# Optimization experiments

Hardware: AMD Instinct MI355X
Metric: run time of the kernel (lower is better)

Reference implementation:

```python
import jax, jax.numpy as jnp
import numpy as np

KSIZE = 3
BJORCK_ITERS = 20
POWER_ITERS = 10


def _power_iteration_sigma(A, u):
    # A: [K, n, n], u: [K, n, 1] -> leading singular value per matrix, [K]
    for _ in range(POWER_ITERS):
        v = jnp.swapaxes(A, -1, -2) @ u
        v = v / jnp.linalg.norm(v, axis=-2, keepdims=True)
        u = A @ v
        u = u / jnp.linalg.norm(u, axis=-2, keepdims=True)
    s = (jnp.swapaxes(u, -1, -2) @ A @ v)[..., 0, 0]
    return s


def _bjorck(w, u):
    # power-iteration scaling is done under no_grad in torch -> stop_gradient
    s = jax.lax.stop_gradient(_power_iteration_sigma(jax.lax.stop_gradient(w), u))
    w = w / s[:, None, None]
    for _ in range(BJORCK_ITERS):
        wtw = jnp.swapaxes(w, -1, -2) @ w
        w = 1.5 * w - 0.5 * (w @ wtw)  # beta = 0.5, first order
    return w


def _block_orth(p1, p2):
    # -> [2, 2, n, n]
    n = p1.shape[0]
    I = jnp.eye(n, dtype=p1.dtype)
    return jnp.stack([
        jnp.stack([p1 @ p2, p1 @ (I - p2)]),
        jnp.stack([(I - p1) @ p2, (I - p1) @ (I - p2)]),
    ])


def _matrix_conv(m1, m2):
    # m1: [k,k,n,n], m2: [l,l,n,n] -> [k+l-1, k+l-1, n, n]
    k, l = m1.shape[0], m2.shape[0]
    size = k + l - 1
    rows = []
    for i in range(size):
        row = []
        for j in range(size):
            acc = 0.0
            for i1 in range(min(k, i + 1)):
                for j1 in range(min(k, j + 1)):
                    if i - i1 < l and j - j1 < l:
                        acc = acc + m1[i1, j1] @ m2[i - i1, j - j1]
            row.append(acc)
        rows.append(jnp.stack(row))
    return jnp.stack(rows)


def _bcop_weight(param_matrices, init_u):
    K, C, _ = param_matrices.shape  # K = 2*(KSIZE-1)+1, C = max_channels
    ortho = _bjorck(param_matrices, init_u)
    H = ortho[0]  # cin == cout == C, full slice
    half = C // 2
    mask = jnp.concatenate(
        [jnp.ones((K - 1, 1, half), ortho.dtype), jnp.zeros((K - 1, 1, C - half), ortho.dtype)],
        axis=-1)
    PQ = ortho[1:] * mask
    PQ = PQ @ jnp.swapaxes(PQ, -1, -2)  # symmetric projections [K-1, C, C]
    p = _block_orth(PQ[0], PQ[1])
    for t in range(1, KSIZE - 1):
        p = _matrix_conv(p, _block_orth(PQ[2 * t], PQ[2 * t + 1]))
    p = jnp.einsum('ab,ijbc->ijac', H, p)  # H @ p[i,j]
    # dict_to_tensor(...).permute(3, 2, 1, 0): [k, k, r, c] -> [c, r, j, i]
    return jnp.transpose(p, (3, 2, 1, 0))  # [C_out, C_in, KSIZE, KSIZE]


def setup_inputs() -> dict:
    key = jax.random.key(0)
    k1, k2, k3, k4 = jax.random.split(key, 4)
    C = 256
    num_kernels = 2 * (KSIZE - 1) + 1
    x = jax.random.normal(k1, (32, C, 64, 64), dtype=jnp.float32)
    param_matrices = jax.random.normal(k2, (num_kernels, C, C), dtype=jnp.float32) / np.sqrt(C)
    init_u = jax.random.normal(k3, (num_kernels, C, 1), dtype=jnp.float32)
    bias = jax.random.uniform(k4, (C,), dtype=jnp.float32, minval=-1.0 / np.sqrt(C), maxval=1.0 / np.sqrt(C))
    return {"x": x, "param_matrices": param_matrices, "init_u": init_u, "bias": bias}


def reference(x, param_matrices, init_u, bias):
    weight = _bcop_weight(param_matrices, init_u)
    # cyclic (circular) padding by k//2 on each side, odd kernel
    pad = KSIZE // 2
    xp = jnp.pad(x, ((0, 0), (0, 0), (pad, pad), (pad, pad)), mode='wrap')
    out = jax.lax.conv_general_dilated(
        xp, weight, window_strides=(1, 1), padding='VALID',
        dimension_numbers=('NCHW', 'OIHW', 'NCHW'))
    return out + bias[None, :, None, None]
```

## Files before the change

kernel.cpp:

```cpp
#include <hip/hip_runtime.h>
#include <stdint.h>

typedef unsigned short u16;
typedef unsigned short u16x4 __attribute__((ext_vector_type(4)));
typedef short bf16x8 __attribute__((ext_vector_type(8)));
typedef float f32x4 __attribute__((ext_vector_type(4)));

#define CDIM 256
#define MSZ 65536

constexpr size_t O_XB   = 0;
constexpr size_t O_AT   = 67108864;
constexpr size_t O_PQH  = 67108864;
constexpr size_t O_PQL  = O_PQH + 524288;
constexpr size_t O_SVAL = 68419584;
constexpr size_t O_W0   = 68419840;
constexpr size_t O_W1   = 71041280;
constexpr size_t O_PH   = 71041280;
constexpr size_t O_PL   = O_PH + 524288;
constexpr size_t O_QTH  = O_PL + 524288;
constexpr size_t O_QTL  = O_QTH + 524288;
constexpr size_t O_TH   = 73662720;
constexpr size_t O_TL   = O_TH + 655360;
constexpr size_t O_RTH  = 74973440;
constexpr size_t O_RTL  = O_RTH + 1179648;
constexpr size_t O_WBQ  = O_RTL + 1179648;

__device__ __forceinline__ u16 f2bf(float f) {
  union { float f; uint32_t u; } a; a.f = f;
  uint32_t u = a.u;
  uint32_t r = u + 0x7FFFu + ((u >> 16) & 1u);
  return (u16)(r >> 16);
}
__device__ __forceinline__ float bf2f(u16 u) {
  union { uint32_t u; float f; } a; a.u = ((uint32_t)u) << 16; return a.f;
}
__device__ __forceinline__ void split_st(u16* hi, u16* lo, float v) {
  u16 h = f2bf(v);
  *hi = h;
  *lo = f2bf(v - bf2f(h));
}
__device__ __forceinline__ void gl16(const void* g, void* l) {
  __builtin_amdgcn_global_load_lds(
      (const __attribute__((address_space(1))) void*)g,
      (__attribute__((address_space(3))) void*)l, 16, 0, 0);
}

__global__ void convert_k(const float* __restrict__ x, u16* __restrict__ xb) {
  __shared__ float t[32][33];
  int b = blockIdx.x;
  int ctile = b & 7, wtile = (b >> 3) & 1, h = (b >> 4) & 63, n = b >> 10;
  int c0 = ctile * 32, w0 = wtile * 32;
  int tid = threadIdx.x;
  for (int p = 0; p < 4; p++) {
    int e = tid + p * 256; int cc = e >> 5, ww = e & 31;
    t[cc][ww] = x[(((size_t)n * 256 + c0 + cc) * 64 + h) * 64 + w0 + ww];
  }
  __syncthreads();
  {
    int ww = tid >> 3, c4 = (tid & 7) * 4;
    u16x4 v;
    #pragma unroll
    for (int j = 0; j < 4; ++j) v[j] = f2bf(t[c4 + j][ww]);
    *(u16x4*)&xb[(((size_t)n * 64 + h) * 64 + w0 + ww) * 256 + c0 + c4] = v;
  }
}

__global__ void wtwA_k(const float* __restrict__ W, float* __restrict__ T) {
  int m = blockIdx.y;
  int i0 = (blockIdx.x >> 3) * 32, j0 = (blockIdx.x & 7) * 32;
  const float* A = W + (size_t)m * MSZ;
  __shared__ float As[32][33], Bs[32][33];
  int tid = threadIdx.x, tx = tid & 15, ty = tid >> 4;
  float a00 = 0, a01 = 0, a10 = 0, a11 = 0;
  for (int kc = 0; kc < CDIM; kc += 32) {
    __syncthreads();
    for (int p = 0; p < 4; p++) {
      int e = tid + p * 256; int kk = e >> 5, cc = e & 31;
      As[kk][cc] = A[(kc + kk) * CDIM + i0 + cc];
      Bs[kk][cc] = A[(kc + kk) * CDIM + j0 + cc];
    }
    __syncthreads();
    #pragma unroll
    for (int kk = 0; kk < 32; kk++) {
      float av0 = As[kk][ty], av1 = As[kk][ty + 16];
      float bv0 = Bs[kk][tx], bv1 = Bs[kk][tx + 16];
      a00 += av0 * bv0; a01 += av0 * bv1; a10 += av1 * bv0; a11 += av1 * bv1;
    }
  }
  float* Tm = T + (size_t)m * MSZ;
  Tm[(i0 + ty) * CDIM + j0 + tx] = a00;
  Tm[(i0 + ty) * CDIM + j0 + tx + 16] = a01;
  Tm[(i0 + ty + 16) * CDIM + j0 + tx] = a10;
  Tm[(i0 + ty + 16) * CDIM + j0 + tx + 16] = a11;
}

__global__ __launch_bounds__(1024) void powerB_k(const float* __restrict__ A,
                                                 const float* __restrict__ B,
                                                 const float* __restrict__ u0,
                                                 float* __restrict__ sval) {
  int m = blockIdx.x;
  int tid = threadIdx.x;
  int t = tid & 255, s = tid >> 8;
  __shared__ float v[256], part[4][257];
  const float* Am = A + (size_t)m * MSZ;
  const float* Bm = B + (size_t)m * MSZ;
  float a = 0.f;
  #pragma unroll 16
  for (int i = 0; i < 64; ++i) a += Am[(s * 64 + i) * 256 + t] * u0[m * 256 + s * 64 + i];
  part[s][t] = a;
  __syncthreads();
  if (s == 0) v[t] = part[0][t] + part[1][t] + part[2][t] + part[3][t];
  __syncthreads();
  for (int it = 0; it < 9; ++it) {
    float b = 0.f;
    #pragma unroll 16
    for (int j = 0; j < 64; ++j) b += Bm[(s * 64 + j) * 256 + t] * v[s * 64 + j];
    part[s][t] = b;
    __syncthreads();
    if (s == 0) v[t] = part[0][t] + part[1][t] + part[2][t] + part[3][t];
    __syncthreads();
  }
  float b = 0.f;
  #pragma unroll 16
  for (int j = 0; j < 64; ++j) b += Bm[(s * 64 + j) * 256 + t] * v[s * 64 + j];
  part[s][t] = b;
  __syncthreads();
  if (s == 0) {
    float w = part[0][t] + part[1][t] + part[2][t] + part[3][t];
    float vv = v[t];
    float d1 = vv * w, d2 = vv * vv;
    for (int off = 32; off; off >>= 1) {
      d1 += __shfl_down(d1, off);
      d2 += __shfl_down(d2, off);
    }
    if ((t & 63) == 0) { part[1][t >> 6] = d1; part[2][t >> 6] = d2; }
  }
  __syncthreads();
  if (tid == 0) {
    float num = part[1][0] + part[1][1] + part[1][2] + part[1][3];
    float den = part[2][0] + part[2][1] + part[2][2] + part[2][3];
    sval[m] = sqrtf(num / den);
  }
}

__global__ void scaleT_k(const float* __restrict__ param, const float* __restrict__ sval,
                         u16* __restrict__ Wh, u16* __restrict__ Wl,
                         u16* __restrict__ Wth, u16* __restrict__ Wtl) {
  __shared__ float tl[32][33];
  int m = blockIdx.y;
  int i0 = (blockIdx.x >> 3) * 32, j0 = (blockIdx.x & 7) * 32;
  int tid = threadIdx.x;
  float inv = 1.0f / sval[m];
  const float* Am = param + (size_t)m * MSZ;
  size_t mo = (size_t)m * MSZ;
  for (int p = 0; p < 4; ++p) {
    int e = tid + p * 256; int ii = e >> 5, jj = e & 31;
    float v = Am[(i0 + ii) * 256 + j0 + jj] * inv;
    tl[ii][jj] = v;
    size_t idx = mo + (size_t)(i0 + ii) * 256 + j0 + jj;
    split_st(&Wh[idx], &Wl[idx], v);
  }
  __syncthreads();
  for (int p = 0; p < 4; ++p) {
    int e = tid + p * 256; int jj = e >> 5, ii = e & 31;
    float v = tl[ii][jj];
    size_t idxT = mo + (size_t)(j0 + jj) * 256 + i0 + ii;
    split_st(&Wth[idxT], &Wtl[idxT], v);
  }
}

__device__ __forceinline__ void gemm32_acc(
    const u16* __restrict__ Ah, const u16* __restrict__ Al, int i0,
    const u16* __restrict__ Bh, const u16* __restrict__ Bl, int j0,
    int K, f32x4* acc, char* smem, int tid)
{
  int lane = tid & 63, wave = tid >> 6;
  int qm = wave >> 1, qn = wave & 1;
  int ra = qm * 16 + (lane & 15);
  int rb = qn * 16 + (lane & 15);
  int kb = (lane >> 4) * 16;
  for (int kc = 0; kc < K; kc += 128) {
    __syncthreads();
    #pragma unroll
    for (int p = 0; p < 8; ++p) {
      int e = tid + p * 256;
      int bufi = e >> 9;
      int r = (e >> 4) & 31;
      int cb = (e & 15) * 16;
      const u16* srcm = (bufi == 0) ? Ah : (bufi == 1) ? Al : (bufi == 2) ? Bh : Bl;
      int r0 = (bufi < 2) ? i0 : j0;
      const char* src = (const char*)srcm + ((size_t)(r0 + r) * 256 + kc) * 2 + cb;
      *(uint4*)(smem + bufi * 8192 + r * 256 + (cb ^ ((r & 7) << 4))) = *(const uint4*)src;
    }
    __syncthreads();
    #pragma unroll
    for (int ks = 0; ks < 4; ++ks) {
      int kbyte = ks * 64 + kb;
      int oa = ra * 256 + (kbyte ^ ((ra & 7) << 4));
      int ob = rb * 256 + (kbyte ^ ((rb & 7) << 4));
      bf16x8 ah = *(const bf16x8*)(smem + oa);
      bf16x8 al = *(const bf16x8*)(smem + 8192 + oa);
      bf16x8 bh = *(const bf16x8*)(smem + 16384 + ob);
      bf16x8 bl = *(const bf16x8*)(smem + 24576 + ob);
      *acc = __builtin_amdgcn_mfma_f32_16x16x32_bf16(ah, bh, *acc, 0, 0, 0);
      *acc = __builtin_amdgcn_mfma_f32_16x16x32_bf16(ah, bl, *acc, 0, 0, 0);
      *acc = __builtin_amdgcn_mfma_f32_16x16x32_bf16(al, bh, *acc, 0, 0, 0);
    }
  }
}

#define GEMM_IDX \
  int tid = threadIdx.x; \
  int lane = tid & 63, wave = tid >> 6, qm = wave >> 1, qn = wave & 1; \
  int orow = qm * 16 + ((lane >> 4) << 2); \
  int ocol = qn * 16 + (lane & 15); \
  int i0 = (blockIdx.x >> 3) * 32, j0 = (blockIdx.x & 7) * 32; \
  __shared__ char smem[32768];

__global__ __launch_bounds__(256) void bjorck_t_k(
    const u16* __restrict__ Wth, const u16* __restrict__ Wtl,
    u16* __restrict__ Th, u16* __restrict__ Tl) {
  GEMM_IDX
  size_t mo = (size_t)blockIdx.y * MSZ;
  f32x4 acc = {};
  gemm32_acc(Wth + mo, Wtl + mo, i0, Wth + mo, Wtl + mo, j0, 256, &acc, smem, tid);
  #pragma unroll
  for (int v = 0; v < 4; ++v) {
    size_t idx = mo + (size_t)(i0 + orow + v) * 256 + (j0 + ocol);
    split_st(&Th[idx], &Tl[idx], acc[v]);
  }
}

__global__ __launch_bounds__(256) void bjorck_u_k(
    const u16* __restrict__ Wh, const u16* __restrict__ Wl,
    const u16* __restrict__ Th, const u16* __restrict__ Tl,
    u16* __restrict__ nWh, u16* __restrict__ nWl,
    u16* __restrict__ nWth, u16* __restrict__ nWtl) {
  GEMM_IDX
  size_t mo = (size_t)blockIdx.y * MSZ;
  f32x4 acc = {};
  gemm32_acc(Wh + mo, Wl + mo, i0, Th + mo, Tl + mo, j0, 256, &acc, smem, tid);
  #pragma unroll
  for (int v = 0; v < 4; ++v) {
    int r = i0 + orow + v, c = j0 + ocol;
    size_t idx = mo + (size_t)r * 256 + c;
    float wv = bf2f(Wh[idx]) + bf2f(Wl[idx]);
    float nv = 1.5f * wv - 0.5f * acc[v];
    split_st(&nWh[idx], &nWl[idx], nv);
    size_t idxT = mo + (size_t)c * 256 + r;
    split_st(&nWth[idxT], &nWtl[idxT], nv);
  }
}

__global__ __launch_bounds__(256) void pq_k(
    const u16* __restrict__ Wh, const u16* __restrict__ Wl,
    u16* __restrict__ PQh, u16* __restrict__ PQl) {
  GEMM_IDX
  int m4 = blockIdx.y;
  const u16* Oh = Wh + (size_t)(1 + m4) * MSZ;
  const u16* Ol = Wl + (size_t)(1 + m4) * MSZ;
  f32x4 acc = {};
  gemm32_acc(Oh, Ol, i0, Oh, Ol, j0, 128, &acc, smem, tid);
  #pragma unroll
  for (int v = 0; v < 4; ++v) {
    size_t idx = (size_t)m4 * MSZ + (size_t)(i0 + orow + v) * 256 + (j0 + ocol);
    split_st(&PQh[idx], &PQl[idx], acc[v]);
  }
}

__global__ __launch_bounds__(256) void c12b_k(
    const u16* __restrict__ PQh, const u16* __restrict__ PQl,
    u16* __restrict__ Ph, u16* __restrict__ Pl,
    u16* __restrict__ QTh, u16* __restrict__ QTl) {
  GEMM_IDX
  f32x4 a1 = {}, a2t = {};
  gemm32_acc(PQh, PQl, i0, PQh + MSZ, PQl + MSZ, j0, 256, &a1, smem, tid);
  gemm32_acc(PQh + 3 * MSZ, PQl + 3 * MSZ, i0, PQh + 2 * MSZ, PQl + 2 * MSZ, j0,
             256, &a2t, smem, tid);
  #pragma unroll
  for (int v = 0; v < 4; ++v) {
    int row = i0 + orow + v, col = j0 + ocol;
    size_t g = (size_t)row * 256 + col;
    float I = (row == col) ? 1.f : 0.f;
    float p0 = bf2f(PQh[g]) + bf2f(PQl[g]);
    float p1 = bf2f(PQh[MSZ + g]) + bf2f(PQl[MSZ + g]);
    float c1 = a1[v];
    split_st(&Ph[g],           &Pl[g],           c1);
    split_st(&Ph[MSZ + g],     &Pl[MSZ + g],     p0 - c1);
    split_st(&Ph[2*MSZ + g],   &Pl[2*MSZ + g],   p1 - c1);
    split_st(&Ph[3*MSZ + g],   &Pl[3*MSZ + g],   I - p0 - p1 + c1);
    float q0 = bf2f(PQh[2*MSZ + g]) + bf2f(PQl[2*MSZ + g]);
    float q1 = bf2f(PQh[3*MSZ + g]) + bf2f(PQl[3*MSZ + g]);
    float c2t = a2t[v];
    split_st(&QTh[g],          &QTl[g],          c2t);
    split_st(&QTh[MSZ + g],    &QTl[MSZ + g],    q0 - c2t);
    split_st(&QTh[2*MSZ + g],  &QTl[2*MSZ + g],  q1 - c2t);
    split_st(&QTh[3*MSZ + g],  &QTl[3*MSZ + g],  I - q0 - q1 + c2t);
  }
}

__global__ __launch_bounds__(256) void mconv_k(
    const u16* __restrict__ Ph, const u16* __restrict__ Pl,
    const u16* __restrict__ QTh, const u16* __restrict__ QTl,
    u16* __restrict__ RTh, u16* __restrict__ RTl) {
  GEMM_IDX
  int ij = blockIdx.y;
  const int toff[10] = {0, 1, 3, 4, 6, 10, 12, 13, 15, 16};
  const int tp[16] = {0, 0, 1, 1, 0, 2, 0, 1, 2, 3, 1, 3, 2, 2, 3, 3};
  const int tq[16] = {0, 1, 0, 1, 2, 0, 3, 2, 1, 0, 3, 1, 2, 3, 2, 3};
  f32x4 acc = {};
  for (int t = toff[ij]; t < toff[ij + 1]; ++t) {
    gemm32_acc(Ph + (size_t)tp[t] * MSZ, Pl + (size_t)tp[t] * MSZ, i0,
               QTh + (size_t)tq[t] * MSZ, QTl + (size_t)tq[t] * MSZ, j0, 256, &acc, smem, tid);
  }
  #pragma unroll
  for (int v = 0; v < 4; ++v) {
    int r = i0 + orow + v, c = j0 + ocol;
    size_t idxT = (size_t)ij * MSZ + (size_t)c * 256 + r;
    split_st(&RTh[idxT], &RTl[idxT], acc[v]);
  }
}

__global__ __launch_bounds__(256) void final_k(
    const u16* __restrict__ Hh, const u16* __restrict__ Hl,
    const u16* __restrict__ RTh, const u16* __restrict__ RTl,
    u16* __restrict__ WBQ) {
  GEMM_IDX
  int ij = blockIdx.y;
  f32x4 acc = {};
  gemm32_acc(Hh, Hl, i0, RTh + (size_t)ij * MSZ, RTl + (size_t)ij * MSZ, j0,
             256, &acc, smem, tid);
  #pragma unroll
  for (int v = 0; v < 4; ++v) {
    int r = i0 + orow + v, c = j0 + ocol;
    int ct = r >> 6, ks = (r >> 5) & 1, jj = (r >> 3) & 3, e = r & 7;
    int s = jj ^ ((c >> 1) & 3);
    int g = ct * 18 + ij * 2 + ks;
    WBQ[(size_t)g * 8192 + (size_t)(c * 4 + s) * 8 + e] = f2bf(acc[v]);
  }
}

__global__ __launch_bounds__(512, 2) void conv_k(
    const u16* __restrict__ xb, const u16* __restrict__ Wb,
    const float* __restrict__ bias, float* __restrict__ out) {
  int braw = blockIdx.x;
  int L = (braw & 7) * 128 + (braw >> 3);
  int h2 = L & 31, n = L >> 5;
  int h0 = h2 * 2;
  int tid = threadIdx.x;
  int lane = tid & 63, wave = tid >> 6;
  int wm = wave >> 2, wn = wave & 3;
  int fr = lane & 15, q = lane >> 4;

  __shared__ char smem[65536];
  char* sX = smem;
  char* sW = smem + 32768;

  f32x4 acc[4][4] = {};

  auto issueX = [&](int ct) {
    #pragma unroll
    for (int i = 0; i < 4; ++i) {
      int d = (wave * 4 + i) * 64 + lane;
      int cb = (d & 7) * 16;
      int w = (d >> 3) & 63;
      int r = d >> 9;
      int hs = (h0 - 1 + r) & 63;
      const char* src = (const char*)xb + (((size_t)(n * 64 + hs) * 64 + w) << 9)
                        + ct * 128 + (cb ^ ((w & 7) << 4));
      gl16(src, sX + (wave * 4 + i) * 1024);
    }
  };
  auto issueW = [&](int g) {
    const char* base = (const char*)Wb + (size_t)g * 16384;
    char* dst = sW + (g & 1) * 16384;
    #pragma unroll
    for (int i = 0; i < 2; ++i) {
      int c = (wave * 2 + i) * 64 + lane;
      gl16(base + c * 16, dst + (wave * 2 + i) * 1024);
    }
  };

  issueX(0);
  issueW(0);
  __syncthreads();

  for (int g = 0; g < 72; ++g) {
    int ct = g / 18, r18 = g % 18, tap = r18 >> 1, ks = r18 & 1;
    int kh = tap % 3, kw = tap / 3;
    if (g + 1 < 72) issueW(g + 1);
    const char* wb = sW + (g & 1) * 16384;
    __builtin_amdgcn_s_setprio(1);
    {
      bf16x8 af[4], bfr[4];
      #pragma unroll
      for (int fn = 0; fn < 4; ++fn) {
        int cl = wn * 64 + fn * 16 + fr;
        bfr[fn] = *(const bf16x8*)(wb + cl * 64 + ((q ^ ((cl >> 1) & 3)) << 4));
      }
      int kb2 = ks * 64 + q * 16;
      #pragma unroll
      for (int fm = 0; fm < 4; ++fm) {
        int wsrc = (fm * 16 + fr + kw + 63) & 63;
        af[fm] = *(const bf16x8*)(sX + ((wm + kh) * 64 + wsrc) * 128 + (kb2 ^ ((wsrc & 7) << 4)));
      }
      #pragma unroll
      for (int fm = 0; fm < 4; ++fm)
        #pragma unroll
        for (int fn = 0; fn < 4; ++fn)
          acc[fm][fn] = __builtin_amdgcn_mfma_f32_16x16x32_bf16(af[fm], bfr[fn], acc[fm][fn], 0, 0, 0);
    }
    __builtin_amdgcn_s_setprio(0);
    if (r18 == 17 && ct < 3) {
      __syncthreads();
      issueX(ct + 1);
      __syncthreads();
    } else {
      __syncthreads();
    }
  }

  __syncthreads();
  float* sF = (float*)smem;
  #pragma unroll
  for (int r = 0; r < 2; ++r) {
    if ((wn >> 1) == r) {
      #pragma unroll
      for (int fn = 0; fn < 4; ++fn) {
        int cl = (wn & 1) * 64 + fn * 16 + fr;
        float bv = bias[r * 128 + cl];
        #pragma unroll
        for (int fm = 0; fm < 4; ++fm) {
          f32x4 v = acc[fm][fn];
          v[0] += bv; v[1] += bv; v[2] += bv; v[3] += bv;
          *(f32x4*)((char*)sF + cl * 512 + wm * 256 +
                    (((unsigned)(fm * 64 + q * 16)) ^ ((unsigned)(cl & 7) << 4))) = v;
        }
      }
    }
    __syncthreads();
    #pragma unroll
    for (int p = 0; p < 8; ++p) {
      int e = tid + p * 512;
      int w4 = e & 15, hloc = (e >> 4) & 1, cl = e >> 5;
      f32x4 val = *(const f32x4*)((const char*)sF + cl * 512 + hloc * 256 +
                                  (((unsigned)(w4 * 16)) ^ ((unsigned)(cl & 7) << 4)));
      *(f32x4*)(out + (((size_t)n * 256 + r * 128 + cl) * 64 + (h0 + hloc)) * 64 + w4 * 4) = val;
    }
    if (r == 0) __syncthreads();
  }
}

extern "C" void kernel_launch(void* const* d_in, const int* in_sizes, int n_in,
                              void* d_out, int out_size, void* d_ws, size_t ws_size,
                              hipStream_t stream) {
  const float* x = (const float*)d_in[0];
  const float* param = (const float*)d_in[1];
  const float* u0 = (const float*)d_in[2];
  const float* bias = (const float*)d_in[3];
  float* out = (float*)d_out;
  char* ws = (char*)d_ws;
  (void)in_sizes; (void)n_in; (void)out_size; (void)ws_size;

  float* B = (float*)(ws + O_AT);
  float* sval = (float*)(ws + O_SVAL);
  u16* W0h  = (u16*)(ws + O_W0);   u16* W0l  = W0h + 327680;
  u16* W0th = W0l + 327680;        u16* W0tl = W0th + 327680;
  u16* W1h  = (u16*)(ws + O_W1);   u16* W1l  = W1h + 327680;
  u16* W1th = W1l + 327680;        u16* W1tl = W1th + 327680;
  u16* Th = (u16*)(ws + O_TH);     u16* Tl = (u16*)(ws + O_TL);
  u16* PQh = (u16*)(ws + O_PQH);   u16* PQl = (u16*)(ws + O_PQL);
  u16* Ph = (u16*)(ws + O_PH);     u16* Pl = (u16*)(ws + O_PL);
  u16* QTh = (u16*)(ws + O_QTH);   u16* QTl = (u16*)(ws + O_QTL);
  u16* RTh = (u16*)(ws + O_RTH);   u16* RTl = (u16*)(ws + O_RTL);
  u16* WBQ = (u16*)(ws + O_WBQ);

  convert_k<<<32768, 256, 0, stream>>>(x, (u16*)(ws + O_XB));
  wtwA_k<<<dim3(64, 5), 256, 0, stream>>>(param, B);
  powerB_k<<<5, 1024, 0, stream>>>(param, B, u0, sval);
  scaleT_k<<<dim3(64, 5), 256, 0, stream>>>(param, sval, W0h, W0l, W0th, W0tl);

  u16 *cWh = W0h, *cWl = W0l, *cWth = W0th, *cWtl = W0tl;
  u16 *nWh = W1h, *nWl = W1l, *nWth = W1th, *nWtl = W1tl;
  for (int it = 0; it < 20; ++it) {
    bjorck_t_k<<<dim3(64, 5), 256, 0, stream>>>(cWth, cWtl, Th, Tl);
    bjorck_u_k<<<dim3(64, 5), 256, 0, stream>>>(cWh, cWl, Th, Tl, nWh, nWl, nWth, nWtl);
    u16* t0;
    t0 = cWh; cWh = nWh; nWh = t0;
    t0 = cWl; cWl = nWl; nWl = t0;
    t0 = cWth; cWth = nWth; nWth = t0;
    t0 = cWtl; cWtl = nWtl; nWtl = t0;
  }

  pq_k<<<dim3(64, 4), 256, 0, stream>>>(cWh, cWl, PQh, PQl);
  c12b_k<<<64, 256, 0, stream>>>(PQh, PQl, Ph, Pl, QTh, QTl);
  mconv_k<<<dim3(64, 9), 256, 0, stream>>>(Ph, Pl, QTh, QTl, RTh, RTl);
  final_k<<<dim3(64, 9), 256, 0, stream>>>(cWh, cWl, RTh, RTl, WBQ);

  conv_k<<<1024, 512, 0, stream>>>((const u16*)(ws + O_XB), WBQ, bias, out);
}
```

Before: 493.4 us.

## Overlap input bf16 conversion with Bjorck iteration GEMM launches

Removes the standalone x-to-bf16 conversion kernel and spreads its 32768 tile blocks across the 40 Bjorck GEMM launches as extra blocks (820 per launch). The Bjorck kernels use only 320 blocks and leave the GPU largely idle, so the memory-bound conversion can fill the unused compute units. The cost is heavier launches whose tail may be set by conversion blocks, which could lengthen the serial Bjorck chain.

After: 451.6 us. 1.09x faster.

```diff
diff --git a/kernel.cpp b/kernel.cpp
--- a/kernel.cpp
+++ b/kernel.cpp
@@ -46,12 +46,13 @@
       (__attribute__((address_space(3))) void*)l, 16, 0, 0);
 }
 
-__global__ void convert_k(const float* __restrict__ x, u16* __restrict__ xb) {
-  __shared__ float t[32][33];
-  int b = blockIdx.x;
+__device__ __forceinline__ void cvt_block(const float* __restrict__ x,
+                                          u16* __restrict__ xb, int b, char* smem) {
+  float (*t)[33] = (float(*)[33])smem;
   int ctile = b & 7, wtile = (b >> 3) & 1, h = (b >> 4) & 63, n = b >> 10;
   int c0 = ctile * 32, w0 = wtile * 32;
   int tid = threadIdx.x;
+  #pragma unroll
   for (int p = 0; p < 4; p++) {
     int e = tid + p * 256; int cc = e >> 5, ww = e & 31;
     t[cc][ww] = x[(((size_t)n * 256 + c0 + cc) * 64 + h) * 64 + w0 + ww];
@@ -220,9 +221,21 @@
 
 __global__ __launch_bounds__(256) void bjorck_t_k(
     const u16* __restrict__ Wth, const u16* __restrict__ Wtl,
-    u16* __restrict__ Th, u16* __restrict__ Tl) {
-  GEMM_IDX
-  size_t mo = (size_t)blockIdx.y * MSZ;
+    u16* __restrict__ Th, u16* __restrict__ Tl,
+    const float* __restrict__ x, u16* __restrict__ xb, int cvt_base) {
+  __shared__ char smem[32768];
+  int bx = blockIdx.x;
+  if (bx >= 320) {
+    int b = cvt_base + bx - 320;
+    if (b < 32768) cvt_block(x, xb, b, smem);
+    return;
+  }
+  int tid = threadIdx.x;
+  int lane = tid & 63, wave = tid >> 6, qm = wave >> 1, qn = wave & 1;
+  int orow = qm * 16 + ((lane >> 4) << 2);
+  int ocol = qn * 16 + (lane & 15);
+  int i0 = ((bx & 63) >> 3) * 32, j0 = (bx & 7) * 32;
+  size_t mo = (size_t)(bx >> 6) * MSZ;
   f32x4 acc = {};
   gemm32_acc(Wth + mo, Wtl + mo, i0, Wth + mo, Wtl + mo, j0, 256, &acc, smem, tid);
   #pragma unroll
@@ -236,9 +249,21 @@
     const u16* __restrict__ Wh, const u16* __restrict__ Wl,
     const u16* __restrict__ Th, const u16* __restrict__ Tl,
     u16* __restrict__ nWh, u16* __restrict__ nWl,
-    u16* __restrict__ nWth, u16* __restrict__ nWtl) {
-  GEMM_IDX
-  size_t mo = (size_t)blockIdx.y * MSZ;
+    u16* __restrict__ nWth, u16* __restrict__ nWtl,
+    const float* __restrict__ x, u16* __restrict__ xb, int cvt_base) {
+  __shared__ char smem[32768];
+  int bx = blockIdx.x;
+  if (bx >= 320) {
+    int b = cvt_base + bx - 320;
+    if (b < 32768) cvt_block(x, xb, b, smem);
+    return;
+  }
+  int tid = threadIdx.x;
+  int lane = tid & 63, wave = tid >> 6, qm = wave >> 1, qn = wave & 1;
+  int orow = qm * 16 + ((lane >> 4) << 2);
+  int ocol = qn * 16 + (lane & 15);
+  int i0 = ((bx & 63) >> 3) * 32, j0 = (bx & 7) * 32;
+  size_t mo = (size_t)(bx >> 6) * MSZ;
   f32x4 acc = {};
   gemm32_acc(Wh + mo, Wl + mo, i0, Th + mo, Tl + mo, j0, 256, &acc, smem, tid);
   #pragma unroll
@@ -465,6 +490,7 @@
 
   float* B = (float*)(ws + O_AT);
   float* sval = (float*)(ws + O_SVAL);
+  u16* xb = (u16*)(ws + O_XB);
   u16* W0h  = (u16*)(ws + O_W0);   u16* W0l  = W0h + 327680;
   u16* W0th = W0l + 327680;        u16* W0tl = W0th + 327680;
   u16* W1h  = (u16*)(ws + O_W1);   u16* W1l  = W1h + 327680;
@@ -476,7 +502,6 @@
   u16* RTh = (u16*)(ws + O_RTH);   u16* RTl = (u16*)(ws + O_RTL);
   u16* WBQ = (u16*)(ws + O_WBQ);
 
-  convert_k<<<32768, 256, 0, stream>>>(x, (u16*)(ws + O_XB));
   wtwA_k<<<dim3(64, 5), 256, 0, stream>>>(param, B);
   powerB_k<<<5, 1024, 0, stream>>>(param, B, u0, sval);
   scaleT_k<<<dim3(64, 5), 256, 0, stream>>>(param, sval, W0h, W0l, W0th, W0tl);
@@ -484,8 +509,10 @@
   u16 *cWh = W0h, *cWl = W0l, *cWth = W0th, *cWtl = W0tl;
   u16 *nWh = W1h, *nWl = W1l, *nWth = W1th, *nWtl = W1tl;
   for (int it = 0; it < 20; ++it) {
-    bjorck_t_k<<<dim3(64, 5), 256, 0, stream>>>(cWth, cWtl, Th, Tl);
-    bjorck_u_k<<<dim3(64, 5), 256, 0, stream>>>(cWh, cWl, Th, Tl, nWh, nWl, nWth, nWtl);
+    bjorck_t_k<<<1140, 256, 0, stream>>>(cWth, cWtl, Th, Tl,
+                                         x, xb, (2 * it) * 820);
+    bjorck_u_k<<<1140, 256, 0, stream>>>(cWh, cWl, Th, Tl, nWh, nWl, nWth, nWtl,
+                                         x, xb, (2 * it + 1) * 820);
     u16* t0;
     t0 = cWh; cWh = nWh; nWh = t0;
     t0 = cWl; cWl = nWl; nWl = t0;
@@ -498,5 +525,5 @@
   mconv_k<<<dim3(64, 9), 256, 0, stream>>>(Ph, Pl, QTh, QTl, RTh, RTl);
   final_k<<<dim3(64, 9), 256, 0, stream>>>(cWh, cWl, RTh, RTl, WBQ);
 
-  conv_k<<<1024, 512, 0, stream>>>((const u16*)(ws + O_XB), WBQ, bias, out);
-}
+  conv_k<<<1024, 512, 0, stream>>>(xb, WBQ, bias, out);
+}
```
